# Kernel optimization log

Measured on AMD Instinct MI355X. Metric: run time of the kernel, lower is better.

Reference implementation:

```python
import jax, jax.numpy as jnp
import numpy as np

T, N, C = 1024, 4, 4
RADIUS, COMPRESSION = 256, 1
TAU = 2.0  # LIF filter time constant (LIF_Filter source unavailable; exponential leaky integrator assumed)


def _build_delay():
    # Mirrors JeffressFilter.__init__ delay construction exactly.
    neg = np.arange(-RADIUS, 0, COMPRESSION, dtype=np.int64)
    pos = np.arange(RADIUS, 0, -COMPRESSION, dtype=np.int64)[::-1]
    _d = np.concatenate([neg, pos]).reshape(-1, 1)            # (D_out, 1)
    delay = np.maximum(np.concatenate([_d, -_d], axis=1), 0)  # relu -> (D_out, 2)
    return jnp.asarray(delay, dtype=jnp.int32)


def setup_inputs() -> dict:
    key = jax.random.key(0)
    k1, k2 = jax.random.split(key)
    x = jax.random.normal(k1, (T, N, C, 2), dtype=jnp.float32)
    delay = _build_delay()                                   # (D_out, 2) int
    d_out = delay.shape[0]                                   # 512
    # get_weight(1.0, 10.0, compression) source unavailable; stand-in float vector per output channel
    weight = jax.random.normal(k2, (d_out,), dtype=jnp.float32)
    return {"x": x, "weight": weight, "delay": delay}


def _lif_filter(x):
    # Leaky integrator over time axis 0: v[t] = exp(-1/tau) * v[t-1] + x[t]
    decay = jnp.asarray(np.exp(-1.0 / TAU), dtype=x.dtype)

    def step(v, xt):
        v = decay * v + xt
        return v, v

    _, y = jax.lax.scan(step, jnp.zeros(x.shape[1:], x.dtype), x)
    return y  # (T, N, C, 2)


def reference(x, weight, delay):
    Tlen = x.shape[0]
    y = _lif_filter(x)                                       # (T, N, C, 2)

    t = jnp.arange(Tlen, dtype=jnp.int32)
    # SpikeDelay.forward: mask rows t >= T - delay to 0, then gather at (t - delay) % T.
    # Equivalent post-gather: out[t] = y[t - delay] if t >= delay else 0 (zero-padded shift).
    t_idx = (t[:, None, None] - delay[None]) % Tlen          # (T, D_out, 2)
    i_idx = jnp.arange(2, dtype=jnp.int32)[None, None, :]    # broadcast over (T, D_out, 2)
    yt = jnp.moveaxis(y, -1, 1)                              # (T, 2, N, C)
    gathered = yt[t_idx, i_idx]                              # (T, D_out, 2, N, C)
    mask = t[:, None, None] >= delay[None]                   # (T, D_out, 2)
    out = jnp.where(mask[..., None, None], gathered, 0.0)
    out = out.sum(axis=2)                                    # sum over in_features=2 -> (T, D_out, N, C)
    out = jnp.moveaxis(out, 1, -1)                           # (T, N, C, D_out)
    return out * weight                                      # scale per output channel
```

## Files before the change

### kernel.cpp

```cpp
#include <hip/hip_runtime.h>


#define T_LEN 1024
#define D_OUT 512

__global__ __launch_bounds__(512) void lif_scan_kernel(const float* __restrict__ x,
                                                       float* __restrict__ y) {
    const int tid   = threadIdx.x;
    const int ch    = tid & 31;
    const int chunk = tid >> 5;
    const int t0    = chunk * 64;
    const float decay = 0.60653065971263342f;

    float v = 0.0f;
    #pragma unroll 8
    for (int k = 0; k < 64; ++k) {
        int t = t0 - 64 + k;
        float xv = (t >= 0) ? x[t * 32 + ch] : 0.0f;
        v = decay * v + xv;
    }
    #pragma unroll 8
    for (int k = 0; k < 64; ++k) {
        int t = t0 + k;
        v = decay * v + x[t * 32 + ch];
        y[t * 32 + ch] = v;
    }
}

__global__ __launch_bounds__(256) void jeffress_kernel(const float* __restrict__ y,
                                                       const float* __restrict__ w,
                                                       const int* __restrict__ delay,
                                                       float4* __restrict__ out) {
    const int f = blockIdx.x * blockDim.x + threadIdx.x;
    const int d4  = f & 127;
    const int tnc = f >> 7;
    const int nc  = tnc & 15;
    const int t   = tnc >> 4;
    const int d   = d4 * 4;

    const int4* dp = (const int4*)(delay + 2 * d);
    const int4 del01 = dp[0];
    const int4 del23 = dp[1];
    const float4 wv = ((const float4*)w)[d4];

    const float* yb = y + nc * 2;

    auto tap = [&](int dl0, int dl1) -> float {
        float a = (t >= dl0) ? yb[(t - dl0) * 32 + 0] : 0.0f;
        float b = (t >= dl1) ? yb[(t - dl1) * 32 + 1] : 0.0f;
        return a + b;
    };

    float4 o;
    o.x = wv.x * tap(del01.x, del01.y);
    o.y = wv.y * tap(del01.z, del01.w);
    o.z = wv.z * tap(del23.x, del23.y);
    o.w = wv.w * tap(del23.z, del23.w);
    out[f] = o;
}

extern "C" void kernel_launch(void* const* d_in, const int* in_sizes, int n_in,
                              void* d_out, int out_size, void* d_ws, size_t ws_size,
                              hipStream_t stream) {
    const float* x      = (const float*)d_in[0];
    const float* weight = (const float*)d_in[1];
    const int*   delay  = (const int*)d_in[2];
    float* out = (float*)d_out;
    float* y   = (float*)d_ws;

    lif_scan_kernel<<<1, 512, 0, stream>>>(x, y);

    const int total4 = T_LEN * 16 * (D_OUT / 4);
    jeffress_kernel<<<total4 / 256, 256, 0, stream>>>(y, weight, delay, (float4*)out);
}
```

Before: 94.25 us.

## Tile jeffress kernel over time with shared-memory window of filtered input

Each block now handles one (n,c) pair and a tile of 16 timesteps. It stages the 272-sample window of the filtered signal into shared memory and computes every delay tap from LDS instead of doing scattered global loads. Each thread writes 8 float4 outputs, and delay and weight loads are amortized across those timesteps. This trades far fewer global gather loads for a sync, some redundant window loading across blocks, and a smaller grid.

```diff
diff --git a/kernel.cpp b/kernel.cpp
--- a/kernel.cpp
+++ b/kernel.cpp
@@ -1,8 +1,10 @@
 #include <hip/hip_runtime.h>
 
 
-#define T_LEN 1024
-#define D_OUT 512
+#define T_LEN  1024
+#define D_OUT  512
+#define T_TILE 16
+#define WIN    (256 + T_TILE)
 
 __global__ __launch_bounds__(512) void lif_scan_kernel(const float* __restrict__ x,
                                                        float* __restrict__ y) {
@@ -31,32 +33,48 @@
                                                        const float* __restrict__ w,
                                                        const int* __restrict__ delay,
                                                        float4* __restrict__ out) {
-    const int f = blockIdx.x * blockDim.x + threadIdx.x;
-    const int d4  = f & 127;
-    const int tnc = f >> 7;
-    const int nc  = tnc & 15;
-    const int t   = tnc >> 4;
-    const int d   = d4 * 4;
+    __shared__ float y0[WIN];
+    __shared__ float y1[WIN];
+
+    const int bid = blockIdx.x;
+    const int nc  = bid & 15;
+    const int t0  = (bid >> 4) * T_TILE;
+    const int tid = threadIdx.x;
+
+    for (int k = tid; k < WIN; k += 256) {
+        const int tg = t0 - 256 + k;
+        float a = 0.0f, b = 0.0f;
+        if (tg >= 0) {
+            const float2 v = *(const float2*)(y + tg * 32 + nc * 2);
+            a = v.x; b = v.y;
+        }
+        y0[k] = a;
+        y1[k] = b;
+    }
+    __syncthreads();
+
+    const int d4 = tid & 127;
+    const int d  = d4 * 4;
+    const int th = tid >> 7;
 
     const int4* dp = (const int4*)(delay + 2 * d);
     const int4 del01 = dp[0];
     const int4 del23 = dp[1];
     const float4 wv = ((const float4*)w)[d4];
 
-    const float* yb = y + nc * 2;
+    float4* outb = out + nc * (D_OUT / 4) + d4;
 
-    auto tap = [&](int dl0, int dl1) -> float {
-        float a = (t >= dl0) ? yb[(t - dl0) * 32 + 0] : 0.0f;
-        float b = (t >= dl1) ? yb[(t - dl1) * 32 + 1] : 0.0f;
-        return a + b;
-    };
-
-    float4 o;
-    o.x = wv.x * tap(del01.x, del01.y);
-    o.y = wv.y * tap(del01.z, del01.w);
-    o.z = wv.z * tap(del23.x, del23.y);
-    o.w = wv.w * tap(del23.z, del23.w);
-    out[f] = o;
+    #pragma unroll
+    for (int j = 0; j < T_TILE / 2; ++j) {
+        const int tl = th * (T_TILE / 2) + j;
+        const int tr = 256 + tl;
+        float4 o;
+        o.x = wv.x * (y0[tr - del01.x] + y1[tr - del01.y]);
+        o.y = wv.y * (y0[tr - del01.z] + y1[tr - del01.w]);
+        o.z = wv.z * (y0[tr - del23.x] + y1[tr - del23.y]);
+        o.w = wv.w * (y0[tr - del23.z] + y1[tr - del23.w]);
+        outb[(t0 + tl) * 16 * (D_OUT / 4)] = o;
+    }
 }
 
 extern "C" void kernel_launch(void* const* d_in, const int* in_sizes, int n_in,
@@ -70,6 +88,6 @@
 
     lif_scan_kernel<<<1, 512, 0, stream>>>(x, y);
 
-    const int total4 = T_LEN * 16 * (D_OUT / 4);
-    jeffress_kernel<<<total4 / 256, 256, 0, stream>>>(y, weight, delay, (float4*)out);
+    const int nblocks = (T_LEN / T_TILE) * 16;
+    jeffress_kernel<<<nblocks, 256, 0, stream>>>(y, weight, delay, (float4*)out);
 }
```

Measured after the change: 81.39 us. 13.6% less time.
